# Optimization experiments

Measured on AMD Instinct MI355X. Metric: run time of the kernel, lower is better.

Reference implementation:

```python
import jax, jax.numpy as jnp
import numpy as np

B, T, V, E, H, M, U, W = 8, 64, 30000, 256, 512, 512, 32, 512


def setup_inputs():
    rng = np.random.RandomState(0)
    ks = jax.random.split(jax.random.key(0), 20)
    u_len = rng.randint(U // 2, U + 1, size=B).astype(np.int32)
    w_len = rng.randint(W // 2, W + 1, size=B).astype(np.int32)
    # word2utt[b, j] = utterance index owning word j; padded words -> last valid utt
    w2u = np.zeros((B, W), np.int32)
    for b in range(B):
        j = np.minimum(np.arange(W), w_len[b] - 1)
        w2u[b] = np.minimum((j * u_len[b]) // w_len[b], u_len[b] - 1)
    s = 0.02
    p = lambda i, shp: jax.random.normal(ks[i], shp, jnp.float32) * s
    emb = p(0, (V, E)).at[0].set(0.0)  # padding_idx=0
    return {
        'target': jax.random.randint(ks[1], (B, T), 0, V, jnp.int32),
        'u_output': jax.random.normal(ks[2], (B, U, M), jnp.float32),
        'w_output': jax.random.normal(ks[3], (B, W, M), jnp.float32),
        'u_len': jnp.asarray(u_len), 'w_len': jnp.asarray(w_len), 'word2utt': jnp.asarray(w2u),
        'emb': emb,
        'W_ih': p(4, (3 * H, E)), 'W_hh': p(5, (3 * H, H)),
        'b_ih': p(6, (3 * H,)), 'b_hh': p(7, (3 * H,)),
        'Wu': p(8, (H, M)), 'bu': p(9, (H,)),
        'Ww': p(10, (H, M)), 'bw': p(11, (H,)),
        'Wo': p(12, (V, H + M)), 'bo': p(13, (V,)),
        'Wd': p(14, (1, V)), 'Wy': p(15, (1, E)),
        'Ws': p(16, (1, H)), 'bs': p(17, (1,)),
    }


def reference(target, u_output, w_output, u_len, w_len, word2utt,
              emb, W_ih, W_hh, b_ih, b_hh, Wu, bu, Ww, bw, Wo, bo, Wd, Wy, Ws, bs):
    Bn = target.shape[0]
    Un = u_output.shape[1]
    Vn = Wo.shape[0]
    Au = jnp.einsum('bum,hm->buh', u_output, Wu) + bu  # attention_u(u_output)
    Aw = jnp.einsum('bwm,hm->bwh', w_output, Ww) + bw  # attention_w(w_output)
    u_mask = jnp.arange(Un)[None, :] < u_len[:, None]               # [B,U]
    w_mask = jnp.arange(w_output.shape[1])[None, :] < w_len[:, None]  # [B,W]
    # initial hidden = last valid utterance state (mem_hidden == dec_hidden)
    h0 = jnp.take_along_axis(u_output, (u_len - 1)[:, None, None], axis=1)[:, 0, :]

    def gru_step(x, h):
        gi = x @ W_ih.T + b_ih
        gh = h @ W_hh.T + b_hh
        ir, iz, inn = jnp.split(gi, 3, axis=-1)
        hr, hz, hn = jnp.split(gh, 3, axis=-1)
        r = jax.nn.sigmoid(ir + hr)
        z = jax.nn.sigmoid(iz + hz)
        n = jnp.tanh(inn + r * hn)
        return (1.0 - z) * n + z * h

    def seg_softmax(sw, seg, valid):  # per-batch ragged per-utterance softmax over words
        swm = jnp.where(valid, sw, -jnp.inf)
        m = jax.ops.segment_max(swm, seg, num_segments=Un)
        e = jnp.where(valid, jnp.exp(sw - m[seg]), 0.0)
        d = jax.ops.segment_sum(e, seg, num_segments=Un)
        return e / d[seg]

    def step(carry, yt):
        h, d_prev, eu_prev = carry
        y = emb[yt]                               # [B,E]
        h_new = gru_step(y, h)                    # rnn_output == new hidden (1 layer)
        su = jnp.einsum('bh,buh->bu', h_new, Au)
        su = jax.nn.softmax(jnp.where(u_mask, su, -jnp.inf), axis=-1)
        gamma = jax.nn.sigmoid(d_prev @ Wd.T + y @ Wy.T + h_new @ Ws.T + bs)  # [B,1]
        su = (1.0 - gamma) * su + gamma * eu_prev
        su = su / jnp.sum(su, axis=-1, keepdims=True)
        sw = jnp.einsum('bh,bwh->bw', h_new, Aw)
        pw = jax.vmap(seg_softmax)(sw, word2utt, w_mask)        # [B,W]
        suw = jnp.take_along_axis(su, word2utt, axis=1) * pw    # [B,W]
        ctx = jnp.einsum('bw,bwm->bm', suw, w_output)
        logits = jnp.concatenate([ctx, h_new], axis=-1) @ Wo.T + bo
        dt = jax.nn.log_softmax(logits, axis=-1)
        return (h_new, dt, su), (dt, suw, su)

    init = (h0, jnp.zeros((Bn, Vn), jnp.float32), jnp.zeros((Bn, Un), jnp.float32))
    _, (dts, suws, sus) = jax.lax.scan(step, init, target.T)
    dec_output = jnp.swapaxes(dts, 0, 1)   # [B,T,V]
    scores_uw = jnp.swapaxes(suws, 0, 1)   # [B,T,W]
    scores_u = jnp.swapaxes(sus, 0, 1)     # [B,T,U]
    return dec_output, scores_uw, scores_u
```

## Files before the change

### kernel.cpp

```cpp
#include <hip/hip_runtime.h>
#include <math.h>

typedef unsigned short ushort_t;
typedef unsigned int uint_t;
typedef unsigned long long ulong_t;
typedef __attribute__((ext_vector_type(8))) short s16x8;
typedef __attribute__((ext_vector_type(4))) float f32x4;

#define BB 8
#define TT 64
#define VV 30000
#define VP 30080
#define EE 256
#define HH 512
#define MM 512
#define UU 32
#define WW 512
#define G3 1536
#define NDB 235
#define NBG 64

#define OFF_GI    0
#define OFF_YALL  786432
#define OFF_WY    917504
#define OFF_H0    918016
#define OFF_HALL  922112
#define OFF_HU    1184256
#define OFF_HW    1446400
#define OFF_HS    1708544
#define OFF_HWV   1709056
#define OFF_P     1709568
#define OFF_SW    1725952
#define OFF_C     1988096
#define OFF_E     6182400
#define OFF_WV    6198784
#define OFF_PART  6200320
#define OFF_LSE   6208512
#define OFF_WOV   6209024
#define OFF_HBT   13909504
#define OFF_SYNC  14040576
#define OFF_PC    14056960

#define DEC_SZ (BB*TT*VV)
#define SUW_OFF DEC_SZ
#define SU_OFF  (DEC_SZ + BB*TT*WW)

__device__ __forceinline__ float sigm(float x){ return 1.0f/(1.0f+__expf(-x)); }
__device__ __forceinline__ ushort_t to_bf16(float f){
  uint_t u = __float_as_uint(f);
  return (ushort_t)((u + 0x7fffu + ((u>>16)&1u)) >> 16);
}


template<int TRANSB>
__global__ void __launch_bounds__(256)
k_gemm_b(const float* __restrict__ A, int lda, int aS,
         const float* __restrict__ B, int ldb, int bS,
         const float* __restrict__ bias,
         float* __restrict__ C, int ldc, int cS, int K){
  A += (size_t)blockIdx.z * aS;
  B += (size_t)blockIdx.z * bS;
  C += (size_t)blockIdx.z * cS;
  __shared__ float As[32][65];
  __shared__ float Bs[32][65];
  int tid = threadIdx.x;
  int bx = blockIdx.x, by = blockIdx.y;
  int tx = tid & 15, ty = tid >> 4;
  float acc[4][4] = {};
  for (int k0 = 0; k0 < K; k0 += 32){
    {
      int r = tid >> 2, cbase = (tid & 3) * 8;
      const float* ap = A + (size_t)(by*64 + r)*lda + k0 + cbase;
      #pragma unroll
      for (int i=0;i<8;++i) As[cbase+i][r] = ap[i];
    }
    if (TRANSB){
      int r = tid >> 2, cbase = (tid & 3) * 8;
      const float* bp = B + (size_t)(bx*64 + r)*ldb + k0 + cbase;
      #pragma unroll
      for (int i=0;i<8;++i) Bs[cbase+i][r] = bp[i];
    } else {
      int kk = tid >> 3, cbase = (tid & 7) * 8;
      const float* bp = B + (size_t)(k0 + kk)*ldb + bx*64 + cbase;
      #pragma unroll
      for (int i=0;i<8;++i) Bs[kk][cbase+i] = bp[i];
    }
    __syncthreads();
    #pragma unroll
    for (int kk=0;kk<32;++kk){
      float a0=As[kk][ty*4+0], a1=As[kk][ty*4+1], a2=As[kk][ty*4+2], a3=As[kk][ty*4+3];
      float b0=Bs[kk][tx*4+0], b1=Bs[kk][tx*4+1], b2=Bs[kk][tx*4+2], b3=Bs[kk][tx*4+3];
      acc[0][0]+=a0*b0; acc[0][1]+=a0*b1; acc[0][2]+=a0*b2; acc[0][3]+=a0*b3;
      acc[1][0]+=a1*b0; acc[1][1]+=a1*b1; acc[1][2]+=a1*b2; acc[1][3]+=a1*b3;
      acc[2][0]+=a2*b0; acc[2][1]+=a2*b1; acc[2][2]+=a2*b2; acc[2][3]+=a2*b3;
      acc[3][0]+=a3*b0; acc[3][1]+=a3*b1; acc[3][2]+=a3*b2; acc[3][3]+=a3*b3;
    }
    __syncthreads();
  }
  #pragma unroll
  for (int i=0;i<4;++i){
    int row = by*64 + ty*4 + i;
    #pragma unroll
    for (int j=0;j<4;++j){
      int col = bx*64 + tx*4 + j;
      float v = acc[i][j];
      if (bias) v += bias[col];
      C[(size_t)row*ldc + col] = v;
    }
  }
}

__global__ void k_y(const int* __restrict__ target, const float* __restrict__ emb,
                    const float* __restrict__ Wy, float* __restrict__ ws){
  int bt = blockIdx.x;
  int e = threadIdx.x;
  __shared__ float r[256];
  int tok = target[bt];
  float v = emb[tok*EE + e];
  ws[OFF_YALL + bt*EE + e] = v;
  r[e] = v * Wy[e];
  __syncthreads();
  for (int s=128; s; s>>=1){ if (e<s) r[e]+=r[e+s]; __syncthreads(); }
  if (e == 0) ws[OFF_WY + bt] = r[0];
}

__global__ void k_h0(const float* __restrict__ u_output, const int* __restrict__ u_len,
                     float* __restrict__ ws){
  int idx = blockIdx.x*256 + threadIdx.x;
  int b = idx >> 9; int k = idx & 511;
  int u = u_len[b]-1;
  ws[OFF_H0 + idx] = u_output[(b*UU+u)*MM + k];
}

__global__ void __launch_bounds__(256)
k_wovc(const float* __restrict__ Wo, ushort_t* __restrict__ wov){
  int idx8 = blockIdx.x*256 + threadIdx.x;
  int v = idx8 >> 6;
  int k8 = (idx8 & 63) << 3;
  uint_t u0=0,u1=0,u2=0,u3=0;
  if (v < VV){
    const float* src = Wo + (size_t)v*1024 + k8;
    float4 f0 = *(const float4*)src;
    float4 f1 = *(const float4*)(src+4);
    u0 = (uint_t)to_bf16(f0.x) | ((uint_t)to_bf16(f0.y) << 16);
    u1 = (uint_t)to_bf16(f0.z) | ((uint_t)to_bf16(f0.w) << 16);
    u2 = (uint_t)to_bf16(f1.x) | ((uint_t)to_bf16(f1.y) << 16);
    u3 = (uint_t)to_bf16(f1.z) | ((uint_t)to_bf16(f1.w) << 16);
  }
  uint4 pk = make_uint4(u0,u1,u2,u3);
  *(uint4*)(wov + (size_t)idx8*8) = pk;
}

__global__ void __launch_bounds__(256)
k_wv(const float* __restrict__ Wo, const float* __restrict__ bo,
     const float* __restrict__ Wd, float* __restrict__ wv){
  __shared__ float wds[128];
  __shared__ float red[256];
  int tid = threadIdx.x;
  int v0 = blockIdx.x*128;
  float pbo=0.f, pwd=0.f;
  if (tid < 128){
    int v = v0 + tid;
    float wd = (v<VV)? Wd[v] : 0.f;
    wds[tid] = wd;
    pbo = wd * ((v<VV)? bo[v] : 0.f);
    pwd = wd;
  }
  __syncthreads();
  float4 acc = {0,0,0,0};
  int nmax = (v0 + 128 <= VV) ? 128 : (VV - v0);
  for (int i=0;i<nmax;++i){
    float wd = wds[i];
    float4 w4 = *(const float4*)(Wo + (size_t)(v0+i)*1024 + tid*4);
    acc.x += wd*w4.x; acc.y += wd*w4.y; acc.z += wd*w4.z; acc.w += wd*w4.w;
  }
  atomicAdd(&wv[tid*4+0], acc.x);
  atomicAdd(&wv[tid*4+1], acc.y);
  atomicAdd(&wv[tid*4+2], acc.z);
  atomicAdd(&wv[tid*4+3], acc.w);
  red[tid] = pbo; __syncthreads();
  for (int s=128; s; s>>=1){ if (tid<s) red[tid]+=red[tid+s]; __syncthreads(); }
  if (tid==0) atomicAdd(&wv[1024], red[0]);
  __syncthreads();
  red[tid] = pwd; __syncthreads();
  for (int s=128; s; s>>=1){ if (tid<s) red[tid]+=red[tid+s]; __syncthreads(); }
  if (tid==0) atomicAdd(&wv[1025], red[0]);
}


__global__ void __launch_bounds__(1024)
k_gru_persist(const float* __restrict__ W_hh, const float* __restrict__ b_hh,
              float* __restrict__ ws){
  uint_t* flags = (uint_t*)(ws + OFF_SYNC);
  int tid  = threadIdx.x;
  int wid  = tid >> 6;
  int lane = tid & 63;
  int half = wid >> 3;
  int kl   = wid & 7;
  int k    = blockIdx.x*8 + kl;
  const float* gi_all = ws + OFF_GI;
  const float* wr = W_hh + (size_t)k*HH;
  const float* wz = W_hh + (size_t)(HH+k)*HH;
  const float* wn = W_hh + (size_t)(2*HH+k)*HH;
  __shared__ float red[16][24];

  for (int t=0; t<TT; ++t){
    const float* hin = (t==0) ? (ws+OFF_H0) : (ws+OFF_HALL + (size_t)(t-1)*4096);
    float* hout = ws + OFF_HALL + (size_t)t*4096;
    float pr[8], pz[8], pn[8];
    #pragma unroll
    for (int b=0;b<8;++b){ pr[b]=0.f; pz[b]=0.f; pn[b]=0.f; }
    int kk0 = half*256 + lane;
    #pragma unroll
    for (int it=0; it<4; ++it){
      int kk = kk0 + it*64;
      float w1 = wr[kk], w2 = wz[kk], w3 = wn[kk];
      #pragma unroll
      for (int b=0;b<8;++b){
        float hv = hin[b*HH+kk];
        pr[b] += hv*w1; pz[b] += hv*w2; pn[b] += hv*w3;
      }
    }
    #pragma unroll
    for (int off=32; off; off>>=1){
      #pragma unroll
      for (int b=0;b<8;++b){
        pr[b] += __shfl_xor(pr[b],off);
        pz[b] += __shfl_xor(pz[b],off);
        pn[b] += __shfl_xor(pn[b],off);
      }
    }
    if (lane == 0){
      #pragma unroll
      for (int b=0;b<8;++b){
        red[wid][b]    = pr[b];
        red[wid][8+b]  = pz[b];
        red[wid][16+b] = pn[b];
      }
    }
    __syncthreads();
    if (tid < 64){
      int klx = tid >> 3, b = tid & 7;
      int k2 = blockIdx.x*8 + klx;
      float prs = red[klx][b]    + red[8+klx][b];
      float pzs = red[klx][8+b]  + red[8+klx][8+b];
      float pns = red[klx][16+b] + red[8+klx][16+b];
      const float* gi = gi_all + (b*TT + t)*G3;
      float r = sigm(gi[k2]      + prs + b_hh[k2]);
      float z = sigm(gi[HH+k2]   + pzs + b_hh[HH+k2]);
      float n = tanhf(gi[2*HH+k2] + r*(pns + b_hh[2*HH+k2]));
      hout[b*HH+k2] = (1.f-z)*n + z*hin[b*HH+k2];
    }
    __syncthreads();
    if (tid == 0)
      __hip_atomic_store(&flags[blockIdx.x*32], (uint_t)(t+1), __ATOMIC_RELEASE, __HIP_MEMORY_SCOPE_AGENT);
    if (tid < NBG){
      while (__hip_atomic_load(&flags[tid*32], __ATOMIC_RELAXED, __HIP_MEMORY_SCOPE_AGENT) < (uint_t)(t+1))
        __builtin_amdgcn_s_sleep(1);
    }
    __syncthreads();
  }
  {
    ushort_t* hbt = (ushort_t*)(ws + OFF_HBT);
    int base = (blockIdx.x*1024 + tid)*4;
    #pragma unroll
    for (int i=0;i<4;++i) hbt[base+i] = to_bf16(ws[OFF_HALL + base + i]);
  }
}


__global__ void __launch_bounds__(256)
k_lh_mfma(const float* __restrict__ Wo, const float* __restrict__ bo,
          const ushort_t* __restrict__ hbt, float* __restrict__ out){
  int tid = threadIdx.x;
  int wv = tid >> 6, l = tid & 63;
  int lm = l & 15, lg = l >> 4;
  int vbase = blockIdx.x*128 + wv*32;
  int rbase = blockIdx.y*128;
  f32x4 acc[2][8];
  #pragma unroll
  for (int s=0;s<2;++s)
    #pragma unroll
    for (int rt=0;rt<8;++rt) acc[s][rt] = (f32x4){0.f,0.f,0.f,0.f};

  for (int k0 = 0; k0 < 512; k0 += 32){
    int kk = k0 + lg*8;
    union { uint_t u[4]; s16x8 s; } af[2];
    #pragma unroll
    for (int s=0;s<2;++s){
      int v = vbase + s*16 + lm; if (v >= VV) v = VV-1;
      const float* ap = Wo + (size_t)v*1024 + 512 + kk;
      float4 f0 = *(const float4*)ap;
      float4 f1 = *(const float4*)(ap+4);
      af[s].u[0] = ((__float_as_uint(f0.x)+0x8000u)>>16) | ((__float_as_uint(f0.y)+0x8000u) & 0xffff0000u);
      af[s].u[1] = ((__float_as_uint(f0.z)+0x8000u)>>16) | ((__float_as_uint(f0.w)+0x8000u) & 0xffff0000u);
      af[s].u[2] = ((__float_as_uint(f1.x)+0x8000u)>>16) | ((__float_as_uint(f1.y)+0x8000u) & 0xffff0000u);
      af[s].u[3] = ((__float_as_uint(f1.z)+0x8000u)>>16) | ((__float_as_uint(f1.w)+0x8000u) & 0xffff0000u);
    }
    #pragma unroll
    for (int rt=0;rt<8;++rt){
      const ushort_t* bp = hbt + (size_t)(rbase + rt*16 + lm)*HH + kk;
      s16x8 bf = *(const s16x8*)bp;
      acc[0][rt] = __builtin_amdgcn_mfma_f32_16x16x32_bf16(af[0].s, bf, acc[0][rt], 0, 0, 0);
      acc[1][rt] = __builtin_amdgcn_mfma_f32_16x16x32_bf16(af[1].s, bf, acc[1][rt], 0, 0, 0);
    }
  }
  float bv[2][4];
  #pragma unroll
  for (int s=0;s<2;++s)
    #pragma unroll
    for (int r=0;r<4;++r){
      int v = vbase + s*16 + lg*4 + r;
      bv[s][r] = (v < VV) ? bo[v] : 0.f;
    }
  #pragma unroll
  for (int rt=0;rt<8;++rt){
    int row = rbase + rt*16 + lm;
    float* orow = out + (size_t)((row&7)*TT + (row>>3))*VV;
    #pragma unroll
    for (int s=0;s<2;++s){
      #pragma unroll
      for (int r=0;r<4;++r){
        int v = vbase + s*16 + lg*4 + r;
        if (v < VV) orow[v] = acc[s][rt][r] + bv[s][r];
      }
    }
  }
}


__global__ void k_hdots(const float* __restrict__ Ws, float* __restrict__ ws){
  int wid  = blockIdx.x*4 + (threadIdx.x>>6);
  int lane = threadIdx.x & 63;
  int row = wid >> 1, which = wid & 1;
  const float* h = ws + OFF_HALL + row*HH;
  const float* src = which ? (ws + OFF_WV + 512) : Ws;
  float acc = 0.f;
  for (int k=lane; k<HH; k+=64) acc += h[k]*src[k];
  for (int off=32; off; off>>=1) acc += __shfl_xor(acc, off);
  if (lane == 0) (which ? ws+OFF_HWV : ws+OFF_HS)[row] = acc;
}

__global__ void k_p(const float* __restrict__ u_output, const int* __restrict__ u_len,
                    float* __restrict__ ws){
  int row = blockIdx.x;
  int b = row & 7;
  int tid = threadIdx.x;
  __shared__ float su_s[UU];
  {
    int u = tid >> 3, l8 = tid & 7;
    const float* hu = ws + OFF_HU + row*512;
    const float* uo = u_output + (size_t)(b*UU + u)*MM;
    float acc = 0.f;
    for (int m=l8; m<MM; m+=8) acc += hu[m]*uo[m];
    acc += __shfl_xor(acc,1); acc += __shfl_xor(acc,2); acc += __shfl_xor(acc,4);
    if (l8 == 0) su_s[u] = acc;
  }
  __syncthreads();
  if (tid < 32){
    int ul = u_len[b];
    float sv = su_s[tid];
    bool valid = tid < ul;
    float mv = valid ? sv : -1e30f;
    for (int off=16; off; off>>=1) mv = fmaxf(mv, __shfl_xor(mv, off));
    float e = valid ? __expf(sv - mv) : 0.f;
    float ssum = e;
    for (int off=16; off; off>>=1) ssum += __shfl_xor(ssum, off);
    ws[OFF_P + row*UU + tid] = e/ssum;
  }
}

__global__ void k_pw(const int* __restrict__ word2utt, const int* __restrict__ w_len,
                     float* __restrict__ ws){
  int row = blockIdx.x;
  int b = row & 7;
  int tid = threadIdx.x;
  __shared__ float sarr[WW];
  __shared__ int   seg[WW];
  __shared__ float marr[UU], darr[UU];
  int wl = w_len[b];
  float* swrow = ws + OFF_SW + row*WW;
  for (int w=tid; w<WW; w+=256){ sarr[w] = swrow[w]; seg[w] = word2utt[b*WW+w]; }
  __syncthreads();
  {
    int g = tid>>3, l8 = tid&7;
    float mv = -1e30f;
    for (int w=l8; w<wl; w+=8) if (seg[w]==g) mv = fmaxf(mv, sarr[w]);
    mv = fmaxf(mv, __shfl_xor(mv,1)); mv = fmaxf(mv, __shfl_xor(mv,2)); mv = fmaxf(mv, __shfl_xor(mv,4));
    float d = 0.f;
    for (int w=l8; w<wl; w+=8) if (seg[w]==g) d += __expf(sarr[w]-mv);
    d += __shfl_xor(d,1); d += __shfl_xor(d,2); d += __shfl_xor(d,4);
    if (l8 == 0){ marr[g]=mv; darr[g]=d; }
  }
  __syncthreads();
  for (int w=tid; w<WW; w+=256){
    float val = 0.f;
    if (w < wl){ int u = seg[w]; val = __expf(sarr[w]-marr[u])/darr[u]; }
    swrow[w] = val;
  }
}

__global__ void __launch_bounds__(256)
k_C(const float* __restrict__ w_output, const int* __restrict__ w_len,
    const int* __restrict__ u_len, const int* __restrict__ word2utt,
    float* __restrict__ ws){
  int row = blockIdx.x;
  int b = row & 7;
  int tid = threadIdx.x;
  __shared__ float pws[WW];
  __shared__ int   seg[WW];
  __shared__ int   st[UU], en[UU];
  __shared__ float wvs[512];
  __shared__ float parr[UU];
  __shared__ float red32[UU][4];
  int wl = w_len[b], ul = u_len[b];
  const float* pwrow = ws + OFF_SW + row*WW;
  for (int w=tid; w<WW; w+=256){ pws[w] = pwrow[w]; seg[w] = word2utt[b*WW+w]; }
  for (int m=tid; m<512; m+=256) wvs[m] = ws[OFF_WV + m];
  if (tid < UU){ st[tid]=0; en[tid]=0; parr[tid] = ws[OFF_P + row*UU + tid]; }
  __syncthreads();
  for (int w=tid; w<wl; w+=256){
    int s = seg[w];
    if (w==0 || seg[w-1]!=s) st[s]=w;
    if (w==wl-1 || seg[w+1]!=s) en[s]=w+1;
  }
  __syncthreads();
  ushort_t* Cu = (ushort_t*)(ws + OFF_C);
  int m0 = tid, m1 = tid + 256;
  int lane = tid & 63, wvi = tid >> 6;
  float pc0 = 0.f, pc1 = 0.f;
  for (int u=0; u<UU; ++u){
    float acc0=0.f, acc1=0.f;
    if (u < ul){
      int s = st[u], e = en[u];
      for (int w=s; w<e; ++w){
        float p = pws[w];
        const float* wo = w_output + ((size_t)(b*WW+w))*MM;
        acc0 += p*wo[m0];
        acc1 += p*wo[m1];
      }
    }
    size_t cbase = ((size_t)row*UU + u)*512;
    Cu[cbase + m0] = to_bf16(acc0);
    Cu[cbase + m1] = to_bf16(acc1);
    float pu = parr[u];
    pc0 += pu*acc0; pc1 += pu*acc1;
    float part = acc0*wvs[m0] + acc1*wvs[m1];
    #pragma unroll
    for (int off=32; off; off>>=1) part += __shfl_xor(part, off);
    if (lane == 0) red32[u][wvi] = part;
  }
  ws[OFF_PC + (size_t)row*512 + m0] = pc0;
  ws[OFF_PC + (size_t)row*512 + m1] = pc1;
  __syncthreads();
  if (tid < UU)
    ws[OFF_E + row*UU + tid] = red32[tid][0]+red32[tid][1]+red32[tid][2]+red32[tid][3];
}


__global__ void __launch_bounds__(512)
k_decode_persist(const int* __restrict__ u_len, const float* __restrict__ bs,
                 const ushort_t* __restrict__ wov,
                 float* __restrict__ ws, float* __restrict__ out){
  int bid = blockIdx.x;
  int tid = threadIdx.x;
  uint_t* sy    = (uint_t*)(ws + OFF_SYNC);
  uint_t* flags = sy + 8192;
  uint_t* go    = sy + 16000;

  if (bid == NDB){
    int wid = tid >> 6, l = tid & 63;
    for (int t=0; t<TT; ++t){
      if (tid < NDB){
        while (__hip_atomic_load(&flags[tid*32], __ATOMIC_RELAXED, __HIP_MEMORY_SCOPE_AGENT) < (uint_t)(t+1))
          __builtin_amdgcn_s_sleep(1);
      }
      __syncthreads();
      {
        const ulong_t* partq = (const ulong_t*)(ws + OFF_PART + (t&1)*4096);
        float ma = -1e30f, sa = 0.f;
        #pragma unroll
        for (int it=0; it<4; ++it){
          int i = l + it*64;
          if (i < NDB){
            ulong_t pq = __hip_atomic_load(&partq[i*8 + wid], __ATOMIC_RELAXED, __HIP_MEMORY_SCOPE_AGENT);
            float m = __uint_as_float((uint_t)pq);
            float s = __uint_as_float((uint_t)(pq >> 32));
            float mm = fmaxf(ma, m);
            sa = sa*__expf(ma-mm) + s*__expf(m-mm);
            ma = mm;
          }
        }
        #pragma unroll
        for (int off=32; off; off>>=1){
          float mo = __shfl_xor(ma, off);
          float so = __shfl_xor(sa, off);
          float mm = fmaxf(ma, mo);
          sa = sa*__expf(ma-mm) + so*__expf(mo-mm);
          ma = mm;
        }
        if (l == 0)
          __hip_atomic_store((float*)(ws + OFF_LSE + t*8 + wid), ma + logf(sa),
                             __ATOMIC_RELAXED, __HIP_MEMORY_SCOPE_AGENT);
      }
      __syncthreads();
      if (tid == 0)
        __hip_atomic_store(go, (uint_t)(t+1), __ATOMIC_RELEASE, __HIP_MEMORY_SCOPE_AGENT);
    }
    return;
  }

  __shared__ float suL[8][32];
  __shared__ float qbufL[8], lseL[8], gamL[8], s2L[8];
  __shared__ int   ulS[8];
  __shared__ uint_t cbPC[16*260];
  __shared__ uint_t cbEC[16*260];
  __shared__ float2 wred[8][8];
  __shared__ float cst[4];
  if (tid == 0){ cst[0]=bs[0]; cst[1]=ws[OFF_WV+1024]; cst[2]=ws[OFF_WV+1025]; }
  if (tid < 8){ qbufL[tid]=0.f; lseL[tid]=0.f; s2L[tid]=1.f; ulS[tid]=u_len[tid]; }
  if (tid < 256) suL[tid>>5][tid&31] = 0.f;
  for (int i=tid; i<8*260; i+=512){ cbPC[8*260 + i] = 0u; cbEC[8*260 + i] = 0u; }
  __syncthreads();

  int wid = tid >> 6, l = tid & 63;
  int lm = l & 15, lgp = l >> 4;
  int vbase = bid*128 + wid*16;
  const ushort_t* ap0 = wov + (size_t)(vbase + lm)*512 + lgp*8;
  const uint_t* cbrowP = cbPC + lm*260 + lgp*4;
  const uint_t* cbrowE = cbEC + lm*260 + lgp*4;

  f32x4 LPC = {0.f,0.f,0.f,0.f};
  f32x4 LEC = {0.f,0.f,0.f,0.f};
  float Lh4[4] = {0.f,0.f,0.f,0.f};

  {
    int b = tid >> 6, l64 = tid & 63;
    const float* PCrow = ws + OFF_PC + (size_t)(b)*512 + l64*8;
    float4 p0 = *(const float4*)PCrow;
    float4 p1 = *(const float4*)(PCrow + 4);
    cbPC[b*260 + l64*4 + 0] = (uint_t)to_bf16(p0.x) | ((uint_t)to_bf16(p0.y) << 16);
    cbPC[b*260 + l64*4 + 1] = (uint_t)to_bf16(p0.z) | ((uint_t)to_bf16(p0.w) << 16);
    cbPC[b*260 + l64*4 + 2] = (uint_t)to_bf16(p1.x) | ((uint_t)to_bf16(p1.y) << 16);
    cbPC[b*260 + l64*4 + 3] = (uint_t)to_bf16(p1.z) | ((uint_t)to_bf16(p1.w) << 16);
  }
  __syncthreads();
  #pragma unroll
  for (int ks=0; ks<16; ++ks){
    s16x8 av = *(const s16x8*)(ap0 + ks*32);
    s16x8 bp = *(const s16x8*)(cbrowP + ks*16);
    LPC = __builtin_amdgcn_mfma_f32_16x16x32_bf16(av, bp, LPC, 0, 0, 0);
  }
  if (lm < 8){
    const float* orow = out + ((size_t)(lm*TT + 0))*VV;
    int vb = vbase + lgp*4;
    #pragma unroll
    for (int r=0;r<4;++r){ int v = vb + r; Lh4[r] = (v < VV) ? orow[v] : 0.f; }
  }

  for (int t=0; t<TT; ++t){
    if (t > 0){
      if (tid == 0){
        while (__hip_atomic_load(go, __ATOMIC_RELAXED, __HIP_MEMORY_SCOPE_AGENT) < (uint_t)t)
          __builtin_amdgcn_s_sleep(1);
      }
      __syncthreads();
      if (tid < 8)
        lseL[tid] = __hip_atomic_load((const float*)(ws + OFF_LSE + (t-1)*8 + tid),
                                      __ATOMIC_RELAXED, __HIP_MEMORY_SCOPE_AGENT);
    }
    __syncthreads();
    if (tid < 8){
      float pd = 0.f;
      if (t > 0)
        pd = qbufL[tid] + ws[OFF_HWV + (t-1)*8 + tid] + cst[1] - lseL[tid]*cst[2];
      gamL[tid] = sigm(pd + ws[OFF_WY + tid*TT + t] + ws[OFF_HS + t*8 + tid] + cst[0]);
    }
    __syncthreads();
    if (tid < 256){
      int b = tid >> 5, j = tid & 31;
      int row = t*8 + b;
      float gg = gamL[b];
      float p = ws[OFF_P + row*UU + j];
      float eu = suL[b][j];
      float mix = (1.f-gg)*p + gg*eu;
      float s2 = mix;
      #pragma unroll
      for (int off=16; off; off>>=1) s2 += __shfl_xor(s2, off);
      float su = mix / s2;
      suL[b][j] = su;
      if (j == 0) s2L[b] = s2;
      float qp = su * ws[OFF_E + row*UU + j];
      #pragma unroll
      for (int off=16; off; off>>=1) qp += __shfl_xor(qp, off);
      if (j == 0) qbufL[b] = qp;
    }
    __syncthreads();
    if (bid < 8 && tid < 32)
      out[SU_OFF + (bid*TT + t)*UU + tid] = suL[bid][tid];

    {
      float pm = -1e30f, ps = 0.f;
      if (lm < 8){
        float gg = gamL[lm];
        float inv = 1.f / s2L[lm];
        float* orow = out + ((size_t)(lm*TT + t))*VV;
        int vb = vbase + lgp*4;
        float l4v[4];
        #pragma unroll
        for (int r=0;r<4;++r)
          l4v[r] = ((1.f-gg)*LPC[r] + gg*LEC[r])*inv + Lh4[r];
        if (vb + 3 < VV){
          *(float4*)(orow + vb) = make_float4(l4v[0],l4v[1],l4v[2],l4v[3]);
        } else {
          #pragma unroll
          for (int r=0;r<4;++r){
            int v = vb + r;
            if (v < VV) orow[v] = l4v[r]; else l4v[r] = -1e30f;
          }
        }
        #pragma unroll
        for (int i=0;i<4;++i) pm = fmaxf(pm, l4v[i]);
        #pragma unroll
        for (int i=0;i<4;++i) ps += (l4v[i] > -5e29f) ? __expf(l4v[i]-pm) : 0.f;
      }
      #pragma unroll
      for (int off=16; off<=32; off<<=1){
        float mo = __shfl_xor(pm, off);
        float so = __shfl_xor(ps, off);
        float nm = fmaxf(pm, mo);
        ps = ps*__expf(pm-nm) + so*__expf(mo-nm);
        pm = nm;
      }
      if (lgp == 0 && lm < 8) wred[wid][lm] = make_float2(pm, ps);
    }
    __syncthreads();
    if (tid < 8){
      float m = -1e30f, s = 0.f;
      #pragma unroll
      for (int w=0; w<8; ++w){
        float2 e = wred[w][tid];
        float nm = fmaxf(m, e.x);
        s = s*__expf(m-nm) + e.y*__expf(e.x-nm);
        m = nm;
      }
      *(float2*)(ws + OFF_PART + (t&1)*4096 + (bid*8 + tid)*2) = make_float2(m, s);
    }
    __syncthreads();
    if (tid == 0)
      __hip_atomic_store(&flags[bid*32], (uint_t)(t+1), __ATOMIC_RELEASE, __HIP_MEMORY_SCOPE_AGENT);

    if (t < TT-1){
      int tn = t + 1;
      {
        int b = tid >> 6, l64 = tid & 63;
        int m8 = l64 * 8;
        int row = tn*8 + b;
        int ul = ulS[b];
        const ushort_t* Crow = (const ushort_t*)(ws + OFF_C) + ((size_t)row*UU)*512 + m8;
        float acc[8];
        #pragma unroll
        for (int i=0;i<8;++i) acc[i]=0.f;
        for (int u=0; u<ul; ++u){
          float su = suL[b][u];
          uint4 c0 = *(const uint4*)(Crow + (size_t)u*512);
          uint_t cc[4] = {c0.x,c0.y,c0.z,c0.w};
          #pragma unroll
          for (int q=0;q<4;++q){
            acc[2*q]   += su * __uint_as_float((cc[q] & 0xffffu) << 16);
            acc[2*q+1] += su * __uint_as_float((cc[q] >> 16) << 16);
          }
        }
        #pragma unroll
        for (int q=0;q<4;++q)
          cbEC[b*260 + l64*4 + q] = (uint_t)to_bf16(acc[2*q]) | ((uint_t)to_bf16(acc[2*q+1]) << 16);
        const float* PCrow = ws + OFF_PC + (size_t)row*512 + m8;
        float4 p0 = *(const float4*)PCrow;
        float4 p1 = *(const float4*)(PCrow + 4);
        cbPC[b*260 + l64*4 + 0] = (uint_t)to_bf16(p0.x) | ((uint_t)to_bf16(p0.y) << 16);
        cbPC[b*260 + l64*4 + 1] = (uint_t)to_bf16(p0.z) | ((uint_t)to_bf16(p0.w) << 16);
        cbPC[b*260 + l64*4 + 2] = (uint_t)to_bf16(p1.x) | ((uint_t)to_bf16(p1.y) << 16);
        cbPC[b*260 + l64*4 + 3] = (uint_t)to_bf16(p1.z) | ((uint_t)to_bf16(p1.w) << 16);
      }
      __syncthreads();
      LPC = (f32x4){0.f,0.f,0.f,0.f};
      LEC = (f32x4){0.f,0.f,0.f,0.f};
      #pragma unroll
      for (int ks=0; ks<16; ++ks){
        s16x8 av = *(const s16x8*)(ap0 + ks*32);
        s16x8 bp = *(const s16x8*)(cbrowP + ks*16);
        s16x8 be = *(const s16x8*)(cbrowE + ks*16);
        LPC = __builtin_amdgcn_mfma_f32_16x16x32_bf16(av, bp, LPC, 0, 0, 0);
        LEC = __builtin_amdgcn_mfma_f32_16x16x32_bf16(av, be, LEC, 0, 0, 0);
      }
      if (lm < 8){
        const float* orow = out + ((size_t)(lm*TT + tn))*VV;
        int vb = vbase + lgp*4;
        #pragma unroll
        for (int r=0;r<4;++r){ int v = vb + r; Lh4[r] = (v < VV) ? orow[v] : 0.f; }
      }
    }
  }
}


__global__ void k_sub2(const float* __restrict__ ws, float* __restrict__ out){
  int v = blockIdx.x*256 + threadIdx.x;
  int tb = blockIdx.y;
  int t = tb >> 3, b = tb & 7;
  if (v < VV) out[(size_t)(b*TT+t)*VV + v] -= ws[OFF_LSE + tb];
}

__global__ void k_suw2(const int* __restrict__ word2utt, const float* __restrict__ ws,
                       float* __restrict__ out){
  int row = blockIdx.x;
  int t = row >> 3, b = row & 7;
  int tid = threadIdx.x;
  for (int w=tid; w<WW; w+=256){
    int seg = word2utt[b*WW + w];
    float su = out[SU_OFF + (b*TT+t)*UU + seg];
    float pw = ws[OFF_SW + row*WW + w];
    out[SUW_OFF + (b*TT+t)*WW + w] = su*pw;
  }
}

extern "C" void kernel_launch(void* const* d_in, const int* in_sizes, int n_in,
                              void* d_out, int out_size, void* d_ws, size_t ws_size,
                              hipStream_t stream) {
  const int*   target   = (const int*)d_in[0];
  const float* u_output = (const float*)d_in[1];
  const float* w_output = (const float*)d_in[2];
  const int*   u_len    = (const int*)d_in[3];
  const int*   w_len    = (const int*)d_in[4];
  const int*   word2utt = (const int*)d_in[5];
  const float* emb      = (const float*)d_in[6];
  const float* W_ih     = (const float*)d_in[7];
  const float* W_hh     = (const float*)d_in[8];
  const float* b_ih     = (const float*)d_in[9];
  const float* b_hh     = (const float*)d_in[10];
  const float* Wu       = (const float*)d_in[11];
  const float* Ww       = (const float*)d_in[13];
  const float* Wo       = (const float*)d_in[15];
  const float* bo       = (const float*)d_in[16];
  const float* Wd       = (const float*)d_in[17];
  const float* Wy       = (const float*)d_in[18];
  const float* Ws       = (const float*)d_in[19];
  const float* bs       = (const float*)d_in[20];
  float* out = (float*)d_out;
  float* ws  = (float*)d_ws;
  ushort_t* wov = (ushort_t*)(ws + OFF_WOV);
  ushort_t* hbt = (ushort_t*)(ws + OFF_HBT);

  hipMemsetAsync(ws + OFF_SYNC, 0, 16384*sizeof(float), stream);

  hipLaunchKernelGGL(k_y, dim3(512), dim3(256), 0, stream, target, emb, Wy, ws);
  hipLaunchKernelGGL((k_gemm_b<1>), dim3(24,8,1), dim3(256), 0, stream,
                     ws+OFF_YALL, 256, 0, W_ih, 256, 0, b_ih, ws+OFF_GI, 1536, 0, 256);
  hipLaunchKernelGGL(k_h0, dim3(16), dim3(256), 0, stream, u_output, u_len, ws);
  hipLaunchKernelGGL(k_wovc, dim3(7520), dim3(256), 0, stream, Wo, wov);
  hipMemsetAsync(ws + OFF_WV, 0, 1536*sizeof(float), stream);
  hipLaunchKernelGGL(k_wv, dim3(235), dim3(256), 0, stream, Wo, bo, Wd, ws+OFF_WV);

  hipLaunchKernelGGL(k_gru_persist, dim3(NBG), dim3(1024), 0, stream, W_hh, b_hh, ws);

  hipLaunchKernelGGL(k_lh_mfma, dim3(235, 4), dim3(256), 0, stream, Wo, bo, hbt, out);
  hipLaunchKernelGGL((k_gemm_b<0>), dim3(8,8,1), dim3(256), 0, stream,
                     ws+OFF_HALL, 512, 0, Wu, 512, 0, (const float*)nullptr, ws+OFF_HU, 512, 0, 512);
  hipLaunchKernelGGL((k_gemm_b<0>), dim3(8,8,1), dim3(256), 0, stream,
                     ws+OFF_HALL, 512, 0, Ww, 512, 0, (const float*)nullptr, ws+OFF_HW, 512, 0, 512);
  hipLaunchKernelGGL(k_hdots, dim3(256), dim3(256), 0, stream, Ws, ws);
  hipLaunchKernelGGL(k_p, dim3(512), dim3(256), 0, stream, u_output, u_len, ws);
  hipLaunchKernelGGL((k_gemm_b<1>), dim3(8,1,8), dim3(256), 0, stream,
                     ws+OFF_HW, 4096, 512, w_output, 512, 262144, (const float*)nullptr,
                     ws+OFF_SW, 4096, 512, 512);
  hipLaunchKernelGGL(k_pw, dim3(512), dim3(256), 0, stream, word2utt, w_len, ws);
  hipLaunchKernelGGL(k_C, dim3(512), dim3(256), 0, stream,
                     w_output, w_len, u_len, word2utt, ws);

  hipLaunchKernelGGL(k_decode_persist, dim3(NDB+1), dim3(512), 0, stream,
                     u_len, bs, wov, ws, out);

  hipLaunchKernelGGL(k_sub2, dim3(118, 512), dim3(256), 0, stream, ws, out);
  hipLaunchKernelGGL(k_suw2, dim3(512), dim3(256), 0, stream, word2utt, ws, out);
}
```

Before: 1.887 ms.

## Move su recurrence and context-expectation into per-batch coordinator blocks

```diff
diff --git a/kernel.cpp b/kernel.cpp
--- a/kernel.cpp
+++ b/kernel.cpp
@@ -40,6 +40,8 @@
 #define OFF_HBT   13909504
 #define OFF_SYNC  14040576
 #define OFF_PC    14056960
+#define OFF_CTXE  14319104
+#define OFF_GS    14323200
 
 #define DEC_SZ (BB*TT*VV)
 #define SUW_OFF DEC_SZ
@@ -467,59 +469,171 @@
   uint_t* sy    = (uint_t*)(ws + OFF_SYNC);
   uint_t* flags = sy + 8192;
   uint_t* go    = sy + 16000;
-
-  if (bid == NDB){
-    int wid = tid >> 6, l = tid & 63;
-    for (int t=0; t<TT; ++t){
+  uint_t* ctxe  = (uint_t*)(ws + OFF_CTXE);
+  float*  gs    = ws + OFF_GS;
+  const ulong_t* partq0 = (const ulong_t*)(ws + OFF_PART);
+  const ulong_t* partq1 = (const ulong_t*)(ws + OFF_PART + 4096);
+
+  if (bid >= NDB){
+    int b = bid - NDB;
+    __shared__ float suLd[UU];
+    __shared__ float gam_s, s2_s, lse_s, qbuf_s;
+    __shared__ float smr[256], ssr[256];
+    float cst0, cst1, cst2;
+    cst0 = bs[0]; cst1 = ws[OFF_WV+1024]; cst2 = ws[OFF_WV+1025];
+    int ul = u_len[b];
+    const ushort_t* Cu = (const ushort_t*)(ws + OFF_C);
+
+    if (tid == 0)
+      gam_s = sigm(ws[OFF_WY + b*TT + 0] + ws[OFF_HS + 0*8 + b] + cst0);
+    __syncthreads();
+    if (tid < 32){
+      float p = ws[OFF_P + (0*8+b)*UU + tid];
+      float mix = (1.f - gam_s)*p;
+      float s2 = mix;
+      #pragma unroll
+      for (int off=16; off; off>>=1) s2 += __shfl_xor(s2, off);
+      float su = mix / s2;
+      suLd[tid] = su;
+      out[SU_OFF + (b*TT + 0)*UU + tid] = su;
+      if (tid == 0) s2_s = s2;
+      float qp = su * ws[OFF_E + (0*8+b)*UU + tid];
+      #pragma unroll
+      for (int off=16; off; off>>=1) qp += __shfl_xor(qp, off);
+      if (tid == 0) qbuf_s = qp;
+    }
+    __syncthreads();
+    if (tid == 0){
+      __hip_atomic_store(&gs[b*2],   gam_s, __ATOMIC_RELAXED, __HIP_MEMORY_SCOPE_AGENT);
+      __hip_atomic_store(&gs[b*2+1], s2_s,  __ATOMIC_RELAXED, __HIP_MEMORY_SCOPE_AGENT);
+    }
+    __syncthreads();
+    if (tid == 0)
+      __hip_atomic_store(&go[b*32], 1u, __ATOMIC_RELEASE, __HIP_MEMORY_SCOPE_AGENT);
+    if (tid < 256){
+      const uint_t* Crow = (const uint_t*)(Cu + ((size_t)(1*8+b)*UU)*512);
+      float a0=0.f, a1=0.f;
+      for (int u=0; u<ul; ++u){
+        uint_t cc = Crow[u*256 + tid];
+        float su = suLd[u];
+        a0 += su * __uint_as_float((cc & 0xffffu) << 16);
+        a1 += su * __uint_as_float((cc >> 16) << 16);
+      }
+      uint_t pk = (uint_t)to_bf16(a0) | ((uint_t)to_bf16(a1) << 16);
+      __hip_atomic_store(&ctxe[(1&1)*2048 + (b<<8) + tid], pk, __ATOMIC_RELAXED, __HIP_MEMORY_SCOPE_AGENT);
+    }
+
+    for (int t=1; t<TT; ++t){
       if (tid < NDB){
-        while (__hip_atomic_load(&flags[tid*32], __ATOMIC_RELAXED, __HIP_MEMORY_SCOPE_AGENT) < (uint_t)(t+1))
+        while (__hip_atomic_load(&flags[tid*32], __ATOMIC_RELAXED, __HIP_MEMORY_SCOPE_AGENT) < (uint_t)t)
           __builtin_amdgcn_s_sleep(1);
       }
       __syncthreads();
       {
-        const ulong_t* partq = (const ulong_t*)(ws + OFF_PART + (t&1)*4096);
-        float ma = -1e30f, sa = 0.f;
+        const ulong_t* pq = ((t-1)&1) ? partq1 : partq0;
+        float m = -1e30f, s = 0.f;
+        if (tid < NDB){
+          ulong_t e = __hip_atomic_load(&pq[tid*8 + b], __ATOMIC_RELAXED, __HIP_MEMORY_SCOPE_AGENT);
+          m = __uint_as_float((uint_t)e);
+          s = __uint_as_float((uint_t)(e >> 32));
+        }
+        if (tid < 256){ smr[tid]=m; ssr[tid]=s; }
+        __syncthreads();
+        if (tid >= 256 && tid < 256+NDB-256+256){}
+        for (int st=128; st; st>>=1){
+          if (tid < st){
+            float m1 = smr[tid], s1 = ssr[tid];
+            float m2 = smr[tid+st], s2 = ssr[tid+st];
+            float mm = fmaxf(m1, m2);
+            ssr[tid] = s1*__expf(m1-mm) + s2*__expf(m2-mm);
+            smr[tid] = mm;
+          }
+          __syncthreads();
+        }
+        if (tid == 0){
+          float lse = smr[0] + logf(ssr[0]);
+          lse_s = lse;
+          __hip_atomic_store((float*)(ws + OFF_LSE + (t-1)*8 + b), lse,
+                             __ATOMIC_RELAXED, __HIP_MEMORY_SCOPE_AGENT);
+        }
+      }
+      __syncthreads();
+      if (tid == 0){
+        float pd = qbuf_s + ws[OFF_HWV + (t-1)*8 + b] + cst1 - lse_s*cst2;
+        gam_s = sigm(pd + ws[OFF_WY + b*TT + t] + ws[OFF_HS + t*8 + b] + cst0);
+      }
+      __syncthreads();
+      if (tid < 32){
+        float p = ws[OFF_P + (t*8+b)*UU + tid];
+        float mix = (1.f - gam_s)*p + gam_s*suLd[tid];
+        float s2 = mix;
         #pragma unroll
-        for (int it=0; it<4; ++it){
-          int i = l + it*64;
-          if (i < NDB){
-            ulong_t pq = __hip_atomic_load(&partq[i*8 + wid], __ATOMIC_RELAXED, __HIP_MEMORY_SCOPE_AGENT);
-            float m = __uint_as_float((uint_t)pq);
-            float s = __uint_as_float((uint_t)(pq >> 32));
-            float mm = fmaxf(ma, m);
-            sa = sa*__expf(ma-mm) + s*__expf(m-mm);
-            ma = mm;
-          }
-        }
+        for (int off=16; off; off>>=1) s2 += __shfl_xor(s2, off);
+        float su = mix / s2;
+        suLd[tid] = su;
+        out[SU_OFF + (b*TT + t)*UU + tid] = su;
+        if (tid == 0) s2_s = s2;
+        float qp = su * ws[OFF_E + (t*8+b)*UU + tid];
         #pragma unroll
-        for (int off=32; off; off>>=1){
-          float mo = __shfl_xor(ma, off);
-          float so = __shfl_xor(sa, off);
-          float mm = fmaxf(ma, mo);
-          sa = sa*__expf(ma-mm) + so*__expf(mo-mm);
-          ma = mm;
-        }
-        if (l == 0)
-          __hip_atomic_store((float*)(ws + OFF_LSE + t*8 + wid), ma + logf(sa),
-                             __ATOMIC_RELAXED, __HIP_MEMORY_SCOPE_AGENT);
+        for (int off=16; off; off>>=1) qp += __shfl_xor(qp, off);
+        if (tid == 0) qbuf_s = qp;
+      }
+      __syncthreads();
+      if (tid == 0){
+        __hip_atomic_store(&gs[b*2],   gam_s, __ATOMIC_RELAXED, __HIP_MEMORY_SCOPE_AGENT);
+        __hip_atomic_store(&gs[b*2+1], s2_s,  __ATOMIC_RELAXED, __HIP_MEMORY_SCOPE_AGENT);
       }
       __syncthreads();
       if (tid == 0)
-        __hip_atomic_store(go, (uint_t)(t+1), __ATOMIC_RELEASE, __HIP_MEMORY_SCOPE_AGENT);
+        __hip_atomic_store(&go[b*32], (uint_t)(t+1), __ATOMIC_RELEASE, __HIP_MEMORY_SCOPE_AGENT);
+      if (t < TT-1 && tid < 256){
+        const uint_t* Crow = (const uint_t*)(Cu + ((size_t)((t+1)*8+b)*UU)*512);
+        float a0=0.f, a1=0.f;
+        for (int u=0; u<ul; ++u){
+          uint_t cc = Crow[u*256 + tid];
+          float su = suLd[u];
+          a0 += su * __uint_as_float((cc & 0xffffu) << 16);
+          a1 += su * __uint_as_float((cc >> 16) << 16);
+        }
+        uint_t pk = (uint_t)to_bf16(a0) | ((uint_t)to_bf16(a1) << 16);
+        __hip_atomic_store(&ctxe[((t+1)&1)*2048 + (b<<8) + tid], pk, __ATOMIC_RELAXED, __HIP_MEMORY_SCOPE_AGENT);
+      }
+    }
+    if (tid < NDB){
+      while (__hip_atomic_load(&flags[tid*32], __ATOMIC_RELAXED, __HIP_MEMORY_SCOPE_AGENT) < (uint_t)TT)
+        __builtin_amdgcn_s_sleep(1);
+    }
+    __syncthreads();
+    {
+      const ulong_t* pq = ((TT-1)&1) ? partq1 : partq0;
+      float m = -1e30f, s = 0.f;
+      if (tid < NDB){
+        ulong_t e = __hip_atomic_load(&pq[tid*8 + b], __ATOMIC_RELAXED, __HIP_MEMORY_SCOPE_AGENT);
+        m = __uint_as_float((uint_t)e);
+        s = __uint_as_float((uint_t)(e >> 32));
+      }
+      if (tid < 256){ smr[tid]=m; ssr[tid]=s; }
+      __syncthreads();
+      for (int st=128; st; st>>=1){
+        if (tid < st){
+          float m1 = smr[tid], s1 = ssr[tid];
+          float m2 = smr[tid+st], s2 = ssr[tid+st];
+          float mm = fmaxf(m1, m2);
+          ssr[tid] = s1*__expf(m1-mm) + s2*__expf(m2-mm);
+          smr[tid] = mm;
+        }
+        __syncthreads();
+      }
+      if (tid == 0)
+        ws[OFF_LSE + (TT-1)*8 + b] = smr[0] + logf(ssr[0]);
     }
     return;
   }
 
-  __shared__ float suL[8][32];
-  __shared__ float qbufL[8], lseL[8], gamL[8], s2L[8];
-  __shared__ int   ulS[8];
+  __shared__ float gamL[8], s2L[8];
   __shared__ uint_t cbPC[16*260];
   __shared__ uint_t cbEC[16*260];
   __shared__ float2 wred[8][8];
-  __shared__ float cst[4];
-  if (tid == 0){ cst[0]=bs[0]; cst[1]=ws[OFF_WV+1024]; cst[2]=ws[OFF_WV+1025]; }
-  if (tid < 8){ qbufL[tid]=0.f; lseL[tid]=0.f; s2L[tid]=1.f; ulS[tid]=u_len[tid]; }
-  if (tid < 256) suL[tid>>5][tid&31] = 0.f;
   for (int i=tid; i<8*260; i+=512){ cbPC[8*260 + i] = 0u; cbEC[8*260 + i] = 0u; }
   __syncthreads();
 
@@ -536,7 +650,7 @@
 
   {
     int b = tid >> 6, l64 = tid & 63;
-    const float* PCrow = ws + OFF_PC + (size_t)(b)*512 + l64*8;
+    const float* PCrow = ws + OFF_PC + (size_t)b*512 + l64*8;
     float4 p0 = *(const float4*)PCrow;
     float4 p1 = *(const float4*)(PCrow + 4);
     cbPC[b*260 + l64*4 + 0] = (uint_t)to_bf16(p0.x) | ((uint_t)to_bf16(p0.y) << 16);
@@ -559,46 +673,32 @@
   }
 
   for (int t=0; t<TT; ++t){
+    if (tid < 8){
+      while (__hip_atomic_load(&go[tid*32], __ATOMIC_RELAXED, __HIP_MEMORY_SCOPE_AGENT) < (uint_t)(t+1))
+        __builtin_amdgcn_s_sleep(1);
+    }
+    __syncthreads();
+    if (tid < 8){
+      gamL[tid] = __hip_atomic_load(&gs[tid*2],   __ATOMIC_RELAXED, __HIP_MEMORY_SCOPE_AGENT);
+      s2L[tid]  = __hip_atomic_load(&gs[tid*2+1], __ATOMIC_RELAXED, __HIP_MEMORY_SCOPE_AGENT);
+    }
     if (t > 0){
-      if (tid == 0){
-        while (__hip_atomic_load(go, __ATOMIC_RELAXED, __HIP_MEMORY_SCOPE_AGENT) < (uint_t)t)
-          __builtin_amdgcn_s_sleep(1);
-      }
-      __syncthreads();
-      if (tid < 8)
-        lseL[tid] = __hip_atomic_load((const float*)(ws + OFF_LSE + (t-1)*8 + tid),
-                                      __ATOMIC_RELAXED, __HIP_MEMORY_SCOPE_AGENT);
-    }
-    __syncthreads();
-    if (tid < 8){
-      float pd = 0.f;
-      if (t > 0)
-        pd = qbufL[tid] + ws[OFF_HWV + (t-1)*8 + tid] + cst[1] - lseL[tid]*cst[2];
-      gamL[tid] = sigm(pd + ws[OFF_WY + tid*TT + t] + ws[OFF_HS + t*8 + tid] + cst[0]);
-    }
-    __syncthreads();
-    if (tid < 256){
-      int b = tid >> 5, j = tid & 31;
-      int row = t*8 + b;
-      float gg = gamL[b];
-      float p = ws[OFF_P + row*UU + j];
-      float eu = suL[b][j];
-      float mix = (1.f-gg)*p + gg*eu;
-      float s2 = mix;
-      #pragma unroll
-      for (int off=16; off; off>>=1) s2 += __shfl_xor(s2, off);
-      float su = mix / s2;
-      suL[b][j] = su;
-      if (j == 0) s2L[b] = s2;
-      float qp = su * ws[OFF_E + row*UU + j];
-      #pragma unroll
-      for (int off=16; off; off>>=1) qp += __shfl_xor(qp, off);
-      if (j == 0) qbufL[b] = qp;
-    }
-    __syncthreads();
-    if (bid < 8 && tid < 32)
-      out[SU_OFF + (bid*TT + t)*UU + tid] = suL[bid][tid];
-
+      int b = tid >> 6, l64 = tid & 63;
+      #pragma unroll
+      for (int q=0;q<4;++q)
+        cbEC[b*260 + l64*4 + q] =
+          __hip_atomic_load(&ctxe[(t&1)*2048 + (b<<8) + l64*4 + q], __ATOMIC_RELAXED, __HIP_MEMORY_SCOPE_AGENT);
+    }
+    __syncthreads();
+    LEC = (f32x4){0.f,0.f,0.f,0.f};
+    if (t > 0){
+      #pragma unroll
+      for (int ks=0; ks<16; ++ks){
+        s16x8 av = *(const s16x8*)(ap0 + ks*32);
+        s16x8 be = *(const s16x8*)(cbrowE + ks*16);
+        LEC = __builtin_amdgcn_mfma_f32_16x16x32_bf16(av, be, LEC, 0, 0, 0);
+      }
+    }
     {
       float pm = -1e30f, ps = 0.f;
       if (lm < 8){
@@ -654,27 +754,7 @@
       int tn = t + 1;
       {
         int b = tid >> 6, l64 = tid & 63;
-        int m8 = l64 * 8;
-        int row = tn*8 + b;
-        int ul = ulS[b];
-        const ushort_t* Crow = (const ushort_t*)(ws + OFF_C) + ((size_t)row*UU)*512 + m8;
-        float acc[8];
-        #pragma unroll
-        for (int i=0;i<8;++i) acc[i]=0.f;
-        for (int u=0; u<ul; ++u){
-          float su = suL[b][u];
-          uint4 c0 = *(const uint4*)(Crow + (size_t)u*512);
-          uint_t cc[4] = {c0.x,c0.y,c0.z,c0.w};
-          #pragma unroll
-          for (int q=0;q<4;++q){
-            acc[2*q]   += su * __uint_as_float((cc[q] & 0xffffu) << 16);
-            acc[2*q+1] += su * __uint_as_float((cc[q] >> 16) << 16);
-          }
-        }
-        #pragma unroll
-        for (int q=0;q<4;++q)
-          cbEC[b*260 + l64*4 + q] = (uint_t)to_bf16(acc[2*q]) | ((uint_t)to_bf16(acc[2*q+1]) << 16);
-        const float* PCrow = ws + OFF_PC + (size_t)row*512 + m8;
+        const float* PCrow = ws + OFF_PC + (size_t)(tn*8+b)*512 + l64*8;
         float4 p0 = *(const float4*)PCrow;
         float4 p1 = *(const float4*)(PCrow + 4);
         cbPC[b*260 + l64*4 + 0] = (uint_t)to_bf16(p0.x) | ((uint_t)to_bf16(p0.y) << 16);
@@ -684,14 +764,11 @@
       }
       __syncthreads();
       LPC = (f32x4){0.f,0.f,0.f,0.f};
-      LEC = (f32x4){0.f,0.f,0.f,0.f};
       #pragma unroll
       for (int ks=0; ks<16; ++ks){
         s16x8 av = *(const s16x8*)(ap0 + ks*32);
         s16x8 bp = *(const s16x8*)(cbrowP + ks*16);
-        s16x8 be = *(const s16x8*)(cbrowE + ks*16);
         LPC = __builtin_amdgcn_mfma_f32_16x16x32_bf16(av, bp, LPC, 0, 0, 0);
-        LEC = __builtin_amdgcn_mfma_f32_16x16x32_bf16(av, be, LEC, 0, 0, 0);
       }
       if (lm < 8){
         const float* orow = out + ((size_t)(lm*TT + tn))*VV;
@@ -777,7 +854,7 @@
   hipLaunchKernelGGL(k_C, dim3(512), dim3(256), 0, stream,
                      w_output, w_len, u_len, word2utt, ws);
 
-  hipLaunchKernelGGL(k_decode_persist, dim3(NDB+1), dim3(512), 0, stream,
+  hipLaunchKernelGGL(k_decode_persist, dim3(NDB+8), dim3(512), 0, stream,
                      u_len, bs, wov, ws, out);
 
   hipLaunchKernelGGL(k_sub2, dim3(118, 512), dim3(256), 0, stream, ws, out);
```

Result: slower. 1.969 ms (+4.4%).

## Fold Wo conversion into GRU helper blocks and fuse LSE subtraction into decode

Applied to the files above, without the earlier changes.

```diff
diff --git a/kernel.cpp b/kernel.cpp
--- a/kernel.cpp
+++ b/kernel.cpp
@@ -19,6 +19,7 @@
 #define G3 1536
 #define NDB 235
 #define NBG 64
+#define NHELP 160
 
 #define OFF_GI    0
 #define OFF_YALL  786432
@@ -132,67 +133,35 @@
   ws[OFF_H0 + idx] = u_output[(b*UU+u)*MM + k];
 }
 
-__global__ void __launch_bounds__(256)
-k_wovc(const float* __restrict__ Wo, ushort_t* __restrict__ wov){
-  int idx8 = blockIdx.x*256 + threadIdx.x;
-  int v = idx8 >> 6;
-  int k8 = (idx8 & 63) << 3;
-  uint_t u0=0,u1=0,u2=0,u3=0;
-  if (v < VV){
-    const float* src = Wo + (size_t)v*1024 + k8;
-    float4 f0 = *(const float4*)src;
-    float4 f1 = *(const float4*)(src+4);
-    u0 = (uint_t)to_bf16(f0.x) | ((uint_t)to_bf16(f0.y) << 16);
-    u1 = (uint_t)to_bf16(f0.z) | ((uint_t)to_bf16(f0.w) << 16);
-    u2 = (uint_t)to_bf16(f1.x) | ((uint_t)to_bf16(f1.y) << 16);
-    u3 = (uint_t)to_bf16(f1.z) | ((uint_t)to_bf16(f1.w) << 16);
-  }
-  uint4 pk = make_uint4(u0,u1,u2,u3);
-  *(uint4*)(wov + (size_t)idx8*8) = pk;
-}
-
-__global__ void __launch_bounds__(256)
-k_wv(const float* __restrict__ Wo, const float* __restrict__ bo,
-     const float* __restrict__ Wd, float* __restrict__ wv){
-  __shared__ float wds[128];
-  __shared__ float red[256];
-  int tid = threadIdx.x;
-  int v0 = blockIdx.x*128;
-  float pbo=0.f, pwd=0.f;
-  if (tid < 128){
-    int v = v0 + tid;
-    float wd = (v<VV)? Wd[v] : 0.f;
-    wds[tid] = wd;
-    pbo = wd * ((v<VV)? bo[v] : 0.f);
-    pwd = wd;
-  }
-  __syncthreads();
-  float4 acc = {0,0,0,0};
-  int nmax = (v0 + 128 <= VV) ? 128 : (VV - v0);
-  for (int i=0;i<nmax;++i){
-    float wd = wds[i];
-    float4 w4 = *(const float4*)(Wo + (size_t)(v0+i)*1024 + tid*4);
-    acc.x += wd*w4.x; acc.y += wd*w4.y; acc.z += wd*w4.z; acc.w += wd*w4.w;
-  }
-  atomicAdd(&wv[tid*4+0], acc.x);
-  atomicAdd(&wv[tid*4+1], acc.y);
-  atomicAdd(&wv[tid*4+2], acc.z);
-  atomicAdd(&wv[tid*4+3], acc.w);
-  red[tid] = pbo; __syncthreads();
-  for (int s=128; s; s>>=1){ if (tid<s) red[tid]+=red[tid+s]; __syncthreads(); }
-  if (tid==0) atomicAdd(&wv[1024], red[0]);
-  __syncthreads();
-  red[tid] = pwd; __syncthreads();
-  for (int s=128; s; s>>=1){ if (tid<s) red[tid]+=red[tid+s]; __syncthreads(); }
-  if (tid==0) atomicAdd(&wv[1025], red[0]);
-}
-
 
 __global__ void __launch_bounds__(1024)
 k_gru_persist(const float* __restrict__ W_hh, const float* __restrict__ b_hh,
-              float* __restrict__ ws){
+              const float* __restrict__ Wo, const float* __restrict__ bo,
+              const float* __restrict__ Wd, float* __restrict__ ws){
+  int tid = threadIdx.x;
+
+  if (blockIdx.x >= NBG){
+    int hb = blockIdx.x - NBG;
+    int k = tid;
+    ushort_t* wovp = (ushort_t*)(ws + OFF_WOV);
+    float* wv = ws + OFF_WV;
+    float wvk = 0.f, pbo = 0.f, pwd = 0.f;
+    for (int v = hb; v < VP; v += NHELP){
+      float w = 0.f, wd = 0.f;
+      if (v < VV){
+        w = Wo[(size_t)v*1024 + k];
+        wd = Wd[v];
+      }
+      if (k < 512) wovp[(size_t)v*512 + k] = to_bf16(w);
+      wvk += w*wd;
+      if (k == 0 && v < VV){ pbo += wd*bo[v]; pwd += wd; }
+    }
+    atomicAdd(&wv[k], wvk);
+    if (k == 0){ atomicAdd(&wv[1024], pbo); atomicAdd(&wv[1025], pwd); }
+    return;
+  }
+
   uint_t* flags = (uint_t*)(ws + OFF_SYNC);
-  int tid  = threadIdx.x;
   int wid  = tid >> 6;
   int lane = tid & 63;
   int half = wid >> 3;
@@ -650,6 +619,22 @@
     if (tid == 0)
       __hip_atomic_store(&flags[bid*32], (uint_t)(t+1), __ATOMIC_RELEASE, __HIP_MEMORY_SCOPE_AGENT);
 
+    if (t > 0 && lm < 8){
+      float ls = lseL[lm];
+      float* orow = out + ((size_t)(lm*TT + (t-1)))*VV;
+      int vb = vbase + lgp*4;
+      if (vb + 3 < VV){
+        float4 o = *(const float4*)(orow + vb);
+        *(float4*)(orow + vb) = make_float4(o.x-ls, o.y-ls, o.z-ls, o.w-ls);
+      } else {
+        #pragma unroll
+        for (int r=0;r<4;++r){
+          int v = vb + r;
+          if (v < VV) orow[v] -= ls;
+        }
+      }
+    }
+
     if (t < TT-1){
       int tn = t + 1;
       {
@@ -701,15 +686,33 @@
       }
     }
   }
-}
-
-
-__global__ void k_sub2(const float* __restrict__ ws, float* __restrict__ out){
-  int v = blockIdx.x*256 + threadIdx.x;
-  int tb = blockIdx.y;
-  int t = tb >> 3, b = tb & 7;
-  if (v < VV) out[(size_t)(b*TT+t)*VV + v] -= ws[OFF_LSE + tb];
-}
+
+  if (tid == 0){
+    while (__hip_atomic_load(go, __ATOMIC_RELAXED, __HIP_MEMORY_SCOPE_AGENT) < (uint_t)TT)
+      __builtin_amdgcn_s_sleep(1);
+  }
+  __syncthreads();
+  if (tid < 8)
+    lseL[tid] = __hip_atomic_load((const float*)(ws + OFF_LSE + (TT-1)*8 + tid),
+                                  __ATOMIC_RELAXED, __HIP_MEMORY_SCOPE_AGENT);
+  __syncthreads();
+  if (lm < 8){
+    float ls = lseL[lm];
+    float* orow = out + ((size_t)(lm*TT + (TT-1)))*VV;
+    int vb = vbase + lgp*4;
+    if (vb + 3 < VV){
+      float4 o = *(const float4*)(orow + vb);
+      *(float4*)(orow + vb) = make_float4(o.x-ls, o.y-ls, o.z-ls, o.w-ls);
+    } else {
+      #pragma unroll
+      for (int r=0;r<4;++r){
+        int v = vb + r;
+        if (v < VV) orow[v] -= ls;
+      }
+    }
+  }
+}
+
 
 __global__ void k_suw2(const int* __restrict__ word2utt, const float* __restrict__ ws,
                        float* __restrict__ out){
@@ -752,16 +755,15 @@
   ushort_t* hbt = (ushort_t*)(ws + OFF_HBT);
 
   hipMemsetAsync(ws + OFF_SYNC, 0, 16384*sizeof(float), stream);
+  hipMemsetAsync(ws + OFF_WV, 0, 1536*sizeof(float), stream);
 
   hipLaunchKernelGGL(k_y, dim3(512), dim3(256), 0, stream, target, emb, Wy, ws);
   hipLaunchKernelGGL((k_gemm_b<1>), dim3(24,8,1), dim3(256), 0, stream,
                      ws+OFF_YALL, 256, 0, W_ih, 256, 0, b_ih, ws+OFF_GI, 1536, 0, 256);
   hipLaunchKernelGGL(k_h0, dim3(16), dim3(256), 0, stream, u_output, u_len, ws);
-  hipLaunchKernelGGL(k_wovc, dim3(7520), dim3(256), 0, stream, Wo, wov);
-  hipMemsetAsync(ws + OFF_WV, 0, 1536*sizeof(float), stream);
-  hipLaunchKernelGGL(k_wv, dim3(235), dim3(256), 0, stream, Wo, bo, Wd, ws+OFF_WV);
-
-  hipLaunchKernelGGL(k_gru_persist, dim3(NBG), dim3(1024), 0, stream, W_hh, b_hh, ws);
+
+  hipLaunchKernelGGL(k_gru_persist, dim3(NBG+NHELP), dim3(1024), 0, stream,
+                     W_hh, b_hh, Wo, bo, Wd, ws);
 
   hipLaunchKernelGGL(k_lh_mfma, dim3(235, 4), dim3(256), 0, stream, Wo, bo, hbt, out);
   hipLaunchKernelGGL((k_gemm_b<0>), dim3(8,8,1), dim3(256), 0, stream,
@@ -780,6 +782,5 @@
   hipLaunchKernelGGL(k_decode_persist, dim3(NDB+1), dim3(512), 0, stream,
                      u_len, bs, wov, ws, out);
 
-  hipLaunchKernelGGL(k_sub2, dim3(118, 512), dim3(256), 0, stream, ws, out);
   hipLaunchKernelGGL(k_suw2, dim3(512), dim3(256), 0, stream, word2utt, ws, out);
 }
```

Measured after the change: 1.887 ms. About the same (-0.0%).
